# Kernel optimization log

Measured on AMD Instinct MI355X. Metric: run time of the kernel, lower is better.

The kernel has to match this reference:

```python
import jax, jax.numpy as jnp
import numpy as np

D_MODEL = 1024
N_HEADS = 16
D_K = D_MODEL // N_HEADS
THETA = 10000.0
SEQ = 2048
BATCH = 2


def setup_inputs() -> dict:
    key = jax.random.key(0)
    ks = jax.random.split(key, 5)
    std = (2.0 / (D_MODEL + D_MODEL)) ** 0.5
    return {
        "x": jax.random.normal(ks[0], (BATCH, SEQ, D_MODEL), dtype=jnp.float32),
        "token_positions": jnp.arange(SEQ, dtype=jnp.int64 if jax.config.jax_enable_x64 else jnp.int32),
        "wq": jax.random.normal(ks[1], (D_MODEL, D_MODEL), dtype=jnp.float32) * std,
        "wk": jax.random.normal(ks[2], (D_MODEL, D_MODEL), dtype=jnp.float32) * std,
        "wv": jax.random.normal(ks[3], (D_MODEL, D_MODEL), dtype=jnp.float32) * std,
        "wo": jax.random.normal(ks[4], (D_MODEL, D_MODEL), dtype=jnp.float32) * std,
    }


def _apply_rope(t, token_positions):
    # t: [b, h, s, d_k]; interleaved even/odd rotation (RoPE)
    k = jnp.arange(D_K // 2, dtype=t.dtype)
    inv_freq = THETA ** (-2.0 * k / D_K)                     # [d_k/2]
    angles = token_positions.astype(t.dtype)[:, None] * inv_freq  # [s, d_k/2]
    cos, sin = jnp.cos(angles), jnp.sin(angles)
    even, odd = t[..., 0::2], t[..., 1::2]
    re = even * cos - odd * sin
    ro = odd * cos + even * sin
    # re-interleave: stack last then reshape back to [..., d_k]
    return jnp.stack([re, ro], axis=-1).reshape(t.shape)


def reference(x, token_positions, wq, wk, wv, wo):
    b, s, _ = x.shape
    def proj(w):
        y = jnp.einsum("bsd,ed->bse", x, w)               # Linear: x @ W^T
        return y.reshape(b, s, N_HEADS, D_K).transpose(0, 2, 1, 3)  # [b,h,s,dk]
    q, k, v = proj(wq), proj(wk), proj(wv)
    q = _apply_rope(q, token_positions)
    k = _apply_rope(k, token_positions)
    scores = jnp.einsum("bhqd,bhkd->bhqk", q, k) / jnp.sqrt(jnp.asarray(D_K, x.dtype))
    attn = jax.nn.softmax(scores, axis=-1)
    out = jnp.einsum("bhqk,bhkd->bhqd", attn, v)          # [b,h,s,dk]
    out = out.transpose(0, 2, 1, 3).reshape(b, s, D_MODEL)
    return jnp.einsum("bsd,ed->bse", out, wo)
```

## Files before the change

### kernel.cpp

```cpp
#include <hip/hip_runtime.h>
#include <stdint.h>

typedef __bf16 bf16x8 __attribute__((ext_vector_type(8)));
typedef __bf16 bf16x2 __attribute__((ext_vector_type(2)));
typedef float f32x4 __attribute__((ext_vector_type(4)));
typedef float f32x16 __attribute__((ext_vector_type(16)));
typedef unsigned short ushort_t;
typedef unsigned int uint;

#define SEQ    2048
#define DMODEL 1024
#define NHEAD  16
#define DKH    64
#define NBATCH 2
#define MROWS  (NBATCH*SEQ)
#define LOG2E  1.44269504088896340736f

__device__ __forceinline__ uint pk2(float a, float b) {
  bf16x2 t; t[0] = (__bf16)a; t[1] = (__bf16)b;
  return __builtin_bit_cast(uint, t);
}
__device__ __forceinline__ ushort_t b1(float a) {
  return __builtin_bit_cast(ushort_t, (__bf16)a);
}
__device__ __forceinline__ float fexp2(float x) {
#if __has_builtin(__builtin_amdgcn_exp2f)
  return __builtin_amdgcn_exp2f(x);
#else
  return exp2f(x);
#endif
}

__device__ __forceinline__ void gload16(const void* g, void* l) {
  __builtin_amdgcn_global_load_lds(
      (const __attribute__((address_space(1))) void*)g,
      (__attribute__((address_space(3))) void*)l, 16, 0, 0);
}

__device__ __forceinline__ f32x4 mfma16(bf16x8 a, bf16x8 b, f32x4 c) {
  return __builtin_amdgcn_mfma_f32_16x16x32_bf16(a, b, c, 0, 0, 0);
}
__device__ __forceinline__ f32x16 mfma32(bf16x8 a, bf16x8 b, f32x16 c) {
  return __builtin_amdgcn_mfma_f32_32x32x16_bf16(a, b, c, 0, 0, 0);
}

__global__ __launch_bounds__(256) void cvt_all(
    const float* __restrict__ x, const float* __restrict__ wq,
    const float* __restrict__ wk, const float* __restrict__ wv,
    const float* __restrict__ wo, uint2* __restrict__ out)
{
  int b = blockIdx.x;
  const float4* src; uint2* dst; int i;
  if (b < 4096) {
    i = b * 256 + threadIdx.x; src = (const float4*)x; dst = out;
  } else {
    int s = (b - 4096) >> 10;
    i = ((b - 4096) & 1023) * 256 + threadIdx.x;
    src = (const float4*)(s == 0 ? wq : s == 1 ? wk : s == 2 ? wv : wo);
    dst = out + (size_t)1048576 + (size_t)s * 262144;
  }
  float4 v = src[i];
  uint2 r; r.x = pk2(v.x, v.y); r.y = pk2(v.z, v.w);
  dst[i] = r;
}

__global__ __launch_bounds__(256) void rope_tab_kernel(const int* __restrict__ tokpos, float2* __restrict__ tab) {
  int t = blockIdx.x * 256 + threadIdx.x;
  int s = t >> 5, k = t & 31;
  double inv = pow(10000.0, -(double)(2 * k) / 64.0);
  double ang = (double)tokpos[s] * inv;
  tab[t] = make_float2((float)cos(ang), (float)sin(ang));
}

__global__ __launch_bounds__(256) void gemm_nt(
    const ushort_t* __restrict__ A, const ushort_t* __restrict__ W,
    const float2* __restrict__ tab,
    ushort_t* __restrict__ Qo, ushort_t* __restrict__ Ko, ushort_t* __restrict__ Vo,
    float* __restrict__ outf, int fused)
{
  __shared__ ushort_t lA[2][128 * 64];
  __shared__ ushort_t lB[2][128 * 64];
  const int tid = threadIdx.x;
  const int w = tid >> 6, l = tid & 63, lo = l & 15, hi = l >> 4;
  const int wr = (w >> 1) * 64, wc = (w & 1) * 64;
  const char* Ab = (const char*)A + (size_t)blockIdx.y * 128 * 2048;
  const char* Bb = (const char*)W + (size_t)blockIdx.x * 128 * 2048;
  f32x4 acc[4][4] = {};

  const int o0 = w * 1024 + l * 16;
  const int r0 = o0 >> 7;
  const int us = ((o0 >> 4) & 7) ^ (r0 & 7);
  const char* ap = Ab + (size_t)r0 * 2048 + us * 16;
  const char* bp = Bb + (size_t)r0 * 2048 + us * 16;

  auto stage = [&](char* dA, char* dB, const char* aq, const char* bq) {
    #pragma unroll
    for (int i = 0; i < 4; ++i) {
      gload16(aq + i * 65536, dA + w * 1024 + i * 4096);
      gload16(bq + i * 65536, dB + w * 1024 + i * 4096);
    }
  };
  auto comp = [&](const ushort_t* lAb, const ushort_t* lBb) {
    #pragma unroll
    for (int c = 0; c < 2; ++c) {
      bf16x8 af[4], wf[4];
      #pragma unroll
      for (int m = 0; m < 4; ++m) {
        int row = wr + m * 16 + lo;
        af[m] = *(const bf16x8*)((const char*)lAb + row * 128 + ((c * 64 + hi * 16) ^ ((row & 7) << 4)));
      }
      #pragma unroll
      for (int n = 0; n < 4; ++n) {
        int row = wc + n * 16 + lo;
        wf[n] = *(const bf16x8*)((const char*)lBb + row * 128 + ((c * 64 + hi * 16) ^ ((row & 7) << 4)));
      }
      #pragma unroll
      for (int m = 0; m < 4; ++m)
        #pragma unroll
        for (int n = 0; n < 4; ++n)
          acc[m][n] = mfma16(af[m], wf[n], acc[m][n]);
    }
  };

  stage((char*)lA[0], (char*)lB[0], ap, bp); ap += 128; bp += 128;
  __syncthreads();
  for (int it = 0; it < 16; it += 2) {
    stage((char*)lA[1], (char*)lB[1], ap, bp); ap += 128; bp += 128;
    comp(lA[0], lB[0]);
    __syncthreads();
    if (it + 2 < 16) { stage((char*)lA[0], (char*)lB[0], ap, bp); ap += 128; bp += 128; }
    comp(lA[1], lB[1]);
    __syncthreads();
  }

  const int mode = fused ? (blockIdx.x >> 3) : 3;
  const int colblk = fused ? (blockIdx.x & 7) : blockIdx.x;
  const int rowbase = blockIdx.y * 128 + wr + hi * 4;
  const int colbase = colblk * 128 + wc + lo;

  if (mode == 3) {
    #pragma unroll
    for (int m = 0; m < 4; ++m)
      #pragma unroll
      for (int n = 0; n < 4; ++n) {
        int e = colbase + n * 16;
        #pragma unroll
        for (int r = 0; r < 4; ++r) {
          int row = rowbase + m * 16 + r;
          outf[(size_t)row * 1024 + e] = acc[m][n][r];
        }
      }
    return;
  }
  if (mode == 2) {
    #pragma unroll
    for (int m = 0; m < 4; ++m) {
      int row0 = rowbase + m * 16;
      int b = row0 >> 11, s = row0 & 2047;
      #pragma unroll
      for (int n = 0; n < 4; ++n) {
        int e = colbase + n * 16;
        int h = e >> 6, dk = e & 63;
        uint2 pk;
        pk.x = pk2(acc[m][n][0], acc[m][n][1]);
        pk.y = pk2(acc[m][n][2], acc[m][n][3]);
        *(uint2*)(Vo + ((size_t)((b * NHEAD + h) * DKH + dk) * SEQ + s)) = pk;
      }
    }
    return;
  }
  ushort_t* outb = (mode == 0) ? Qo : Ko;
  const float qscale = (mode == 0) ? (0.125f * LOG2E) : 1.0f;
  #pragma unroll
  for (int m = 0; m < 4; ++m) {
    #pragma unroll
    for (int n = 0; n < 4; ++n) {
      int e = colbase + n * 16;
      int h = e >> 6, dk = e & 63, kf = dk >> 1;
      float sgn = (e & 1) ? 1.0f : -1.0f;
      #pragma unroll
      for (int r = 0; r < 4; ++r) {
        int row = rowbase + m * 16 + r;
        int s = row & 2047, b = row >> 11;
        float2 cs = tab[s * 32 + kf];
        float v = acc[m][n][r];
        float p = __shfl_xor(v, 1, 64);
        float res = (v * cs.x + sgn * p * cs.y) * qscale;
        outb[((size_t)((b * NHEAD + h) * SEQ + s)) * DKH + dk] = b1(res);
      }
    }
  }
}

__global__ __launch_bounds__(128) void attn_fwd(
    const ushort_t* __restrict__ Qg, const ushort_t* __restrict__ Kg,
    const ushort_t* __restrict__ VTg, ushort_t* __restrict__ attn)
{
  __shared__ char lds[49152];
  const int tid = threadIdx.x;
  const int w = tid >> 6, l = tid & 63;
  const int q31 = l & 31, hf = l >> 5, s7 = l & 7;
  const int bh = blockIdx.y;
  const int q0 = blockIdx.x * 128 + w * 64;
  const char* Kb = (const char*)Kg + (size_t)bh * 2048 * 128;
  const char* Vb = (const char*)VTg + (size_t)bh * 64 * 4096;

  bf16x8 qreg[2][4];
  #pragma unroll
  for (int qb = 0; qb < 2; ++qb) {
    const ushort_t* qp = Qg + ((size_t)bh * 2048 + q0 + qb * 32 + q31) * 64 + hf * 8;
    #pragma unroll
    for (int c = 0; c < 4; ++c) qreg[qb][c] = *(const bf16x8*)(qp + c * 16);
  }

  f32x16 accO[2][2] = {};
  float lsum[2] = {0.f, 0.f};

  const char* ra[4];
  #pragma unroll
  for (int c = 0; c < 4; ++c)
    ra[c] = lds + q31 * 128 + ((c * 32 + hf * 16) ^ (s7 << 4));
  const int lPoff = 32768 + w * 8192;
  char* wbase = lds + lPoff + q31 * 128 + hf * 8;

  const int su = (tid & 7) ^ ((tid >> 3) & 7);
  const char* kp = Kb + (size_t)(tid >> 3) * 128 + su * 16;
  const char* vp = Vb + (size_t)(tid >> 3) * 4096 + su * 16;

  auto stage = [&](char* base, const char* kq, const char* vq) {
    #pragma unroll
    for (int i = 0; i < 4; ++i)
      gload16(kq + i * 2048, base + i * 2048 + tid * 16);
    #pragma unroll
    for (int i = 0; i < 4; ++i)
      gload16(vq + i * 65536, base + 8192 + i * 2048 + tid * 16);
  };

  auto tile = [&](int bo) {
    #pragma unroll
    for (int kb = 0; kb < 2; ++kb) {
      bf16x8 kf[4];
      #pragma unroll
      for (int c = 0; c < 4; ++c)
        kf[c] = *(const bf16x8*)(ra[c] + bo + kb * 4096);
      #pragma unroll
      for (int qb = 0; qb < 2; ++qb) {
        f32x16 s = {};
        #pragma unroll
        for (int c = 0; c < 4; ++c) s = mfma32(kf[c], qreg[qb][c], s);
        float p[16];
        float ts = 0.f;
        #pragma unroll
        for (int r = 0; r < 16; ++r) { p[r] = fexp2(s[r]); ts += p[r]; }
        lsum[qb] += ts;
        #pragma unroll
        for (int g2 = 0; g2 < 4; ++g2) {
          uint2 pk;
          pk.x = pk2(p[g2 * 4 + 0], p[g2 * 4 + 1]);
          pk.y = pk2(p[g2 * 4 + 2], p[g2 * 4 + 3]);
          *(uint2*)(wbase + qb * 4096 + ((kb * 64 + g2 * 16) ^ (s7 << 4))) = pk;
        }
      }
      #pragma unroll
      for (int kcl = 0; kcl < 2; ++kcl) {
        int kc = kb * 2 + kcl;
        bf16x8 vf0 = *(const bf16x8*)(ra[kc] + bo + 8192);
        bf16x8 vf1 = *(const bf16x8*)(ra[kc] + bo + 8192 + 4096);
        #pragma unroll
        for (int qb = 0; qb < 2; ++qb) {
          bf16x8 pb = *(const bf16x8*)(ra[kc] + lPoff + qb * 4096);
          accO[qb][0] = mfma32(vf0, pb, accO[qb][0]);
          accO[qb][1] = mfma32(vf1, pb, accO[qb][1]);
        }
      }
    }
  };

  stage(lds, kp, vp); kp += 8192; vp += 128;
  for (int kt = 0; kt < 32; kt += 2) {
    __syncthreads();
    stage(lds + 16384, kp, vp); kp += 8192; vp += 128;
    tile(0);
    __syncthreads();
    if (kt + 2 < 32) { stage(lds, kp, vp); kp += 8192; vp += 128; }
    tile(16384);
  }

  int b = bh >> 4, head = bh & 15;
  #pragma unroll
  for (int qb = 0; qb < 2; ++qb) {
    float lt = lsum[qb] + __shfl_xor(lsum[qb], 32, 64);
    float inv = 1.0f / lt;
    ushort_t* op = attn + (size_t)(b * 2048 + q0 + qb * 32 + q31) * 1024 + head * 64;
    #pragma unroll
    for (int db = 0; db < 2; ++db)
      #pragma unroll
      for (int m = 0; m < 4; ++m) {
        int d0 = db * 32 + m * 8 + hf * 4;
        uint2 pk;
        pk.x = pk2(accO[qb][db][m * 4 + 0] * inv, accO[qb][db][m * 4 + 1] * inv);
        pk.y = pk2(accO[qb][db][m * 4 + 2] * inv, accO[qb][db][m * 4 + 3] * inv);
        *(uint2*)(op + d0) = pk;
      }
  }
}

extern "C" void kernel_launch(void* const* d_in, const int* in_sizes, int n_in,
                              void* d_out, int out_size, void* d_ws, size_t ws_size,
                              hipStream_t stream) {
  const float* x  = (const float*)d_in[0];
  const int* tok  = (const int*)d_in[1];
  const float* wq = (const float*)d_in[2];
  const float* wk = (const float*)d_in[3];
  const float* wv = (const float*)d_in[4];
  const float* wo = (const float*)d_in[5];
  float* out = (float*)d_out;
  char* ws = (char*)d_ws;

  size_t off = 0;
  float2* tab = (float2*)(ws + off); off += (size_t)SEQ * 32 * sizeof(float2);
  ushort_t* xb  = (ushort_t*)(ws + off); off += (size_t)MROWS * DMODEL * 2;
  ushort_t* wqkv = (ushort_t*)(ws + off); off += (size_t)3 * DMODEL * DMODEL * 2;
  ushort_t* wob = (ushort_t*)(ws + off); off += (size_t)DMODEL * DMODEL * 2;
  ushort_t* Qg  = (ushort_t*)(ws + off); off += (size_t)MROWS * DMODEL * 2;
  ushort_t* Kg  = (ushort_t*)(ws + off); off += (size_t)MROWS * DMODEL * 2;
  ushort_t* VTg = (ushort_t*)(ws + off); off += (size_t)MROWS * DMODEL * 2;
  ushort_t* attnb = xb;
  if (ws_size < off) return;

  cvt_all<<<8192, 256, 0, stream>>>(x, wq, wk, wv, wo, (uint2*)xb);
  rope_tab_kernel<<<256, 256, 0, stream>>>(tok, tab);

  gemm_nt<<<dim3(24, 32), 256, 0, stream>>>(xb, wqkv, tab, Qg, Kg, VTg, nullptr, 1);

  attn_fwd<<<dim3(SEQ / 128, NBATCH * NHEAD), 128, 0, stream>>>(Qg, Kg, VTg, attnb);

  gemm_nt<<<dim3(8, 32), 256, 0, stream>>>(attnb, wob, nullptr, nullptr, nullptr, nullptr, out, 0);
}
```

Baseline: 134.3 us.

## Triple-buffer K/V tiles in attention with explicit vmcnt waits and barriers

```diff
diff --git a/kernel.cpp b/kernel.cpp
--- a/kernel.cpp
+++ b/kernel.cpp
@@ -196,7 +196,7 @@
     const ushort_t* __restrict__ Qg, const ushort_t* __restrict__ Kg,
     const ushort_t* __restrict__ VTg, ushort_t* __restrict__ attn)
 {
-  __shared__ char lds[49152];
+  __shared__ char lds[65536];
   const int tid = threadIdx.x;
   const int w = tid >> 6, l = tid & 63;
   const int q31 = l & 31, hf = l >> 5, s7 = l & 7;
@@ -220,71 +220,93 @@
   #pragma unroll
   for (int c = 0; c < 4; ++c)
     ra[c] = lds + q31 * 128 + ((c * 32 + hf * 16) ^ (s7 << 4));
-  const int lPoff = 32768 + w * 8192;
+  const int lPoff = 49152 + w * 8192;
   char* wbase = lds + lPoff + q31 * 128 + hf * 8;
 
   const int su = (tid & 7) ^ ((tid >> 3) & 7);
   const char* kp = Kb + (size_t)(tid >> 3) * 128 + su * 16;
   const char* vp = Vb + (size_t)(tid >> 3) * 4096 + su * 16;
 
-  auto stage = [&](char* base, const char* kq, const char* vq) {
+  auto stageT = [&](int bufo) {
     #pragma unroll
     for (int i = 0; i < 4; ++i)
-      gload16(kq + i * 2048, base + i * 2048 + tid * 16);
+      gload16(kp + i * 2048, lds + bufo + i * 2048 + tid * 16);
     #pragma unroll
     for (int i = 0; i < 4; ++i)
-      gload16(vq + i * 65536, base + 8192 + i * 2048 + tid * 16);
+      gload16(vp + i * 65536, lds + bufo + 8192 + i * 2048 + tid * 16);
+    kp += 8192; vp += 128;
   };
 
-  auto tile = [&](int bo) {
+  auto tileC = [&](int bo) {
     #pragma unroll
     for (int kb = 0; kb < 2; ++kb) {
       bf16x8 kf[4];
       #pragma unroll
       for (int c = 0; c < 4; ++c)
         kf[c] = *(const bf16x8*)(ra[c] + bo + kb * 4096);
-      #pragma unroll
-      for (int qb = 0; qb < 2; ++qb) {
-        f32x16 s = {};
-        #pragma unroll
-        for (int c = 0; c < 4; ++c) s = mfma32(kf[c], qreg[qb][c], s);
-        float p[16];
-        float ts = 0.f;
-        #pragma unroll
-        for (int r = 0; r < 16; ++r) { p[r] = fexp2(s[r]); ts += p[r]; }
-        lsum[qb] += ts;
-        #pragma unroll
-        for (int g2 = 0; g2 < 4; ++g2) {
-          uint2 pk;
-          pk.x = pk2(p[g2 * 4 + 0], p[g2 * 4 + 1]);
-          pk.y = pk2(p[g2 * 4 + 2], p[g2 * 4 + 3]);
-          *(uint2*)(wbase + qb * 4096 + ((kb * 64 + g2 * 16) ^ (s7 << 4))) = pk;
-        }
+      f32x16 s0 = {}, s1 = {};
+      #pragma unroll
+      for (int c = 0; c < 4; ++c) {
+        s0 = mfma32(kf[c], qreg[0][c], s0);
+        s1 = mfma32(kf[c], qreg[1][c], s1);
+      }
+      float p0[16], p1[16];
+      float t0 = 0.f, t1 = 0.f;
+      #pragma unroll
+      for (int r = 0; r < 16; ++r) { p0[r] = fexp2(s0[r]); t0 += p0[r]; }
+      #pragma unroll
+      for (int r = 0; r < 16; ++r) { p1[r] = fexp2(s1[r]); t1 += p1[r]; }
+      lsum[0] += t0; lsum[1] += t1;
+      #pragma unroll
+      for (int g2 = 0; g2 < 4; ++g2) {
+        uint2 pk;
+        pk.x = pk2(p0[g2 * 4 + 0], p0[g2 * 4 + 1]);
+        pk.y = pk2(p0[g2 * 4 + 2], p0[g2 * 4 + 3]);
+        *(uint2*)(wbase + ((kb * 64 + g2 * 16) ^ (s7 << 4))) = pk;
+      }
+      #pragma unroll
+      for (int g2 = 0; g2 < 4; ++g2) {
+        uint2 pk;
+        pk.x = pk2(p1[g2 * 4 + 0], p1[g2 * 4 + 1]);
+        pk.y = pk2(p1[g2 * 4 + 2], p1[g2 * 4 + 3]);
+        *(uint2*)(wbase + 4096 + ((kb * 64 + g2 * 16) ^ (s7 << 4))) = pk;
       }
       #pragma unroll
       for (int kcl = 0; kcl < 2; ++kcl) {
         int kc = kb * 2 + kcl;
         bf16x8 vf0 = *(const bf16x8*)(ra[kc] + bo + 8192);
         bf16x8 vf1 = *(const bf16x8*)(ra[kc] + bo + 8192 + 4096);
-        #pragma unroll
-        for (int qb = 0; qb < 2; ++qb) {
-          bf16x8 pb = *(const bf16x8*)(ra[kc] + lPoff + qb * 4096);
-          accO[qb][0] = mfma32(vf0, pb, accO[qb][0]);
-          accO[qb][1] = mfma32(vf1, pb, accO[qb][1]);
-        }
+        bf16x8 pb0 = *(const bf16x8*)(ra[kc] + lPoff);
+        bf16x8 pb1 = *(const bf16x8*)(ra[kc] + lPoff + 4096);
+        accO[0][0] = mfma32(vf0, pb0, accO[0][0]);
+        accO[0][1] = mfma32(vf1, pb0, accO[0][1]);
+        accO[1][0] = mfma32(vf0, pb1, accO[1][0]);
+        accO[1][1] = mfma32(vf1, pb1, accO[1][1]);
       }
     }
   };
 
-  stage(lds, kp, vp); kp += 8192; vp += 128;
-  for (int kt = 0; kt < 32; kt += 2) {
-    __syncthreads();
-    stage(lds + 16384, kp, vp); kp += 8192; vp += 128;
-    tile(0);
-    __syncthreads();
-    if (kt + 2 < 32) { stage(lds, kp, vp); kp += 8192; vp += 128; }
-    tile(16384);
-  }
+  stageT(0);
+  stageT(16384);
+  #pragma unroll 1
+  for (int it = 0; it < 10; ++it) {
+    #pragma unroll
+    for (int j = 0; j < 3; ++j) {
+      asm volatile("s_waitcnt vmcnt(8)" ::: "memory");
+      __builtin_amdgcn_s_barrier();
+      __builtin_amdgcn_sched_barrier(0);
+      stageT(((j + 2) % 3) * 16384);
+      tileC(j * 16384);
+    }
+  }
+  asm volatile("s_waitcnt vmcnt(8)" ::: "memory");
+  __builtin_amdgcn_s_barrier();
+  __builtin_amdgcn_sched_barrier(0);
+  tileC(0);
+  asm volatile("s_waitcnt vmcnt(0)" ::: "memory");
+  __builtin_amdgcn_s_barrier();
+  __builtin_amdgcn_sched_barrier(0);
+  tileC(16384);
 
   int b = bh >> 4, head = bh & 15;
   #pragma unroll
```

Measured after the change: 133.0 us. No clear change (-1.0%).
